# Optimization experiments

Measured on AMD Instinct MI355X. Metric: run time of the kernel, lower is better.

## Reference

```python
import jax, jax.numpy as jnp
import numpy as np

EPS = 1e-12

def _l2n(x):
    # torch F.normalize(p=2, dim=0): x / max(||x||_2, eps)
    return x / jnp.maximum(jnp.linalg.norm(x), EPS)

def _gru_cell(x, h, Wi, Wh, bi, bh):
    # torch GRU cell math; Wi:(3H,Din), Wh:(3H,H)
    gi = Wi @ x + bi
    gh = Wh @ h + bh
    i_r, i_z, i_n = jnp.split(gi, 3)
    h_r, h_z, h_n = jnp.split(gh, 3)
    r = jax.nn.sigmoid(i_r + h_r)
    z = jax.nn.sigmoid(i_z + h_z)
    n = jnp.tanh(i_n + r * h_n)
    return (1.0 - z) * n + z * h

def setup_inputs() -> dict:
    key = jax.random.key(0)
    ks = jax.random.split(key, 20)
    m, n, T = 10, 10, 100
    H1, H2, HID = 1600, 400, 2000
    D_in, D_out = 2 * m + n, m * n
    f32 = jnp.float32
    inp = {
        'y': jax.random.normal(ks[0], (n, T), f32),
        'm1x_0': jax.random.normal(ks[1], (m,), f32),
        'F': jax.random.normal(ks[2], (m, m), f32) * 0.1,
        'Hm': jax.random.normal(ks[3], (n, m), f32) * 0.1,
        'h0': jax.random.normal(ks[4], (2, HID), f32),
        'W1': jax.random.normal(ks[5], (H1, D_in), f32) * 0.05,
        'b1': jax.random.normal(ks[6], (H1,), f32) * 0.05,
        'Wi0': jax.random.normal(ks[7], (3 * HID, H1), f32) * 0.02,
        'Wh0': jax.random.normal(ks[8], (3 * HID, HID), f32) * 0.02,
        'bi0': jax.random.normal(ks[9], (3 * HID,), f32) * 0.02,
        'bh0': jax.random.normal(ks[10], (3 * HID,), f32) * 0.02,
        'Wi1': jax.random.normal(ks[11], (3 * HID, HID), f32) * 0.02,
        'Wh1': jax.random.normal(ks[12], (3 * HID, HID), f32) * 0.02,
        'bi1': jax.random.normal(ks[13], (3 * HID,), f32) * 0.02,
        'bh1': jax.random.normal(ks[14], (3 * HID,), f32) * 0.02,
        'W2': jax.random.normal(ks[15], (H2, HID), f32) * 0.02,
        'b2': jax.random.normal(ks[16], (H2,), f32) * 0.02,
        'W3': jax.random.normal(ks[17], (D_out, H2), f32) * 0.01,
        'b3': jax.random.normal(ks[18], (D_out,), f32) * 0.01,
    }
    return inp

def reference(y, m1x_0, F, Hm, h0, W1, b1, Wi0, Wh0, bi0, bh0,
              Wi1, Wh1, bi1, bh1, W2, b2, W3, b3):
    n, T = y.shape
    m = m1x_0.shape[0]
    # first step uses obs_process_0 = h(f(m1x_0)) as y_previous surrogate
    y_prev0 = Hm @ (F @ m1x_0)
    carry0 = (m1x_0, jnp.zeros_like(m1x_0), m1x_0, y_prev0, h0[0], h0[1])

    def step(carry, yt):
        post, prev_post, prev_prior, y_prev, h1, h2 = carry
        prior = F @ post              # step_prior
        m1y = Hm @ prior
        f1 = _l2n(yt - y_prev)        # innovation diff feature
        f3 = _l2n(post - prev_post)   # posterior update feature
        f4 = _l2n(post - prev_prior)  # residual feature
        kin = jnp.concatenate([f1, f3, f4])  # (2m+n,)
        a = jax.nn.relu(W1 @ kin + b1)
        h1n = _gru_cell(a, h1, Wi0, Wh0, bi0, bh0)
        h2n = _gru_cell(h1n, h2, Wi1, Wh1, bi1, bh1)
        g = jax.nn.relu(W2 @ h2n + b2)
        KG = (W3 @ g + b3).reshape(m, n)
        dy = yt - m1y
        new_post = prior + KG @ dy
        return (new_post, post, prior, yt, h1n, h2n), new_post

    _, xs = jax.lax.scan(step, carry0, y.T)  # xs: (T, m)
    return xs.T  # (m, T)
```

## Files before the change

### kernel.cpp

```cpp
#include <hip/hip_runtime.h>
#include <math.h>

#define NB 256
#define NT 1024
#define NW 16
#define TT 100
#define MM 10
#define NN 10
#define HID 2000
#define H1 1600
#define H2 400
#define G3 6000
#define KP 2048
#define RPB 24

#define SCOPE_AGENT __HIP_MEMORY_SCOPE_AGENT

typedef _Float16 h2v __attribute__((ext_vector_type(2)));

__device__ __forceinline__ float sigf(float x) { return 1.f / (1.f + __expf(-x)); }
__device__ __forceinline__ float tanhfast(float x) { return 2.f / (1.f + __expf(-2.f * x)) - 1.f; }

__device__ __forceinline__ float ld_coh(const float* p) {
  return __hip_atomic_load(p, __ATOMIC_RELAXED, SCOPE_AGENT);
}
__device__ __forceinline__ void st_coh(float* p, float v) {
  __hip_atomic_store(p, v, __ATOMIC_RELAXED, SCOPE_AGENT);
}
__device__ __forceinline__ float2 ld_coh2(const float* p) {
  unsigned long long v = __hip_atomic_load((const unsigned long long*)p,
                                           __ATOMIC_RELAXED, SCOPE_AGENT);
  union { unsigned long long u; float2 f; } c; c.u = v; return c.f;
}
__device__ __forceinline__ void stage_coh(const float* __restrict__ src,
                                          float* __restrict__ dst, int n, int tid) {
  const int n2 = n >> 1;
  for (int j = tid; j < n2; j += NT) {
    float2 v = ld_coh2(src + 2 * j);
    dst[2 * j]     = v.x;
    dst[2 * j + 1] = v.y;
  }
}

__device__ __forceinline__ void gridbar(unsigned* flags, unsigned* release,
                                        unsigned ep, int tid, int blk) {
  __syncthreads();
  if (tid == 0)
    __hip_atomic_store(flags + blk * 16, ep, __ATOMIC_RELAXED, SCOPE_AGENT);
  if (blk == 0) {
    if (tid < NB) {
      while (__hip_atomic_load(flags + tid * 16, __ATOMIC_RELAXED, SCOPE_AGENT) < ep)
        __builtin_amdgcn_s_sleep(1);
    }
    __syncthreads();
    if (tid == 0)
      __hip_atomic_store(release, ep, __ATOMIC_RELAXED, SCOPE_AGENT);
  } else {
    if (tid == 0) {
      while (__hip_atomic_load(release, __ATOMIC_RELAXED, SCOPE_AGENT) < ep)
        __builtin_amdgcn_s_sleep(1);
    }
  }
  __syncthreads();
}

__device__ __forceinline__ void set_flag(unsigned* f, unsigned v, int tid) {
  __syncthreads();
  if (tid == 0) __hip_atomic_store(f, v, __ATOMIC_RELAXED, SCOPE_AGENT);
}
__device__ __forceinline__ void wait_flag(const unsigned* f, unsigned v, int tid) {
  if (tid == 0) {
    while (__hip_atomic_load(f, __ATOMIC_RELAXED, SCOPE_AGENT) < v)
      __builtin_amdgcn_s_sleep(1);
  }
  __syncthreads();
}

template<int K>
__device__ __forceinline__ float rowdotT(const float* __restrict__ row,
                                         const float* __restrict__ x, int ln) {
  constexpr int NFULL = K / 256;
  constexpr int REM   = K - NFULL * 256;
  const int base = ln * 4;
  float4 w[NFULL + (REM ? 1 : 0)];
  #pragma unroll
  for (int i = 0; i < NFULL; ++i)
    w[i] = *reinterpret_cast<const float4*>(row + base + i * 256);
  bool tail = false;
  if constexpr (REM != 0) {
    tail = (base + NFULL * 256 + 3 < K);
    if (tail) w[NFULL] = *reinterpret_cast<const float4*>(row + base + NFULL * 256);
  }
  float acc = 0.f;
  #pragma unroll
  for (int i = 0; i < NFULL; ++i) {
    const float4 xv = *reinterpret_cast<const float4*>(x + base + i * 256);
    acc = fmaf(w[i].x, xv.x, acc);
    acc = fmaf(w[i].y, xv.y, acc);
    acc = fmaf(w[i].z, xv.z, acc);
    acc = fmaf(w[i].w, xv.w, acc);
  }
  if constexpr (REM != 0) {
    if (tail) {
      const float4 xv = *reinterpret_cast<const float4*>(x + base + NFULL * 256);
      acc = fmaf(w[NFULL].x, xv.x, acc);
      acc = fmaf(w[NFULL].y, xv.y, acc);
      acc = fmaf(w[NFULL].z, xv.z, acc);
      acc = fmaf(w[NFULL].w, xv.w, acc);
    }
  }
  #pragma unroll
  for (int off = 32; off; off >>= 1) acc += __shfl_xor(acc, off, 64);
  return acc;
}

__device__ __forceinline__ void sweep24(const _Float16* __restrict__ W,
                                        const float* __restrict__ bias,
                                        int row0, int nrows,
                                        const _Float16* __restrict__ xh,
                                        float* __restrict__ outw,
                                        bool relu,
                                        int wv, int ln, int tid, float* red,
                                        float* __restrict__ gloc)
{
  const _Float16* wp = W + (size_t)row0 * KP + wv * 3072 + ln * 8;
  uint4 w[6];
  #pragma unroll
  for (int c = 0; c < 6; ++c)
    w[c] = *reinterpret_cast<const uint4*>(wp + c * 512);
  float a0 = 0.f, a1 = 0.f;
  const int first = (3 * wv) >> 1;
  #pragma unroll
  for (int c = 0; c < 6; ++c) {
    const int flat = wv * 3072 + c * 512;
    const int sel  = (flat >> 11) - first;
    const int col  = (flat & (KP - 1)) + ln * 8;
    const uint4 xv = *reinterpret_cast<const uint4*>(xh + col);
    union { uint4 u; h2v h[4]; } wu, xu;
    wu.u = w[c]; xu.u = xv;
    float acc = sel ? a1 : a0;
    #pragma unroll
    for (int q = 0; q < 4; ++q)
      acc = __builtin_amdgcn_fdot2(wu.h[q], xu.h[q], acc, false);
    if (sel) a1 = acc; else a0 = acc;
  }
  #pragma unroll
  for (int off = 32; off; off >>= 1) {
    a0 += __shfl_xor(a0, off, 64);
    a1 += __shfl_xor(a1, off, 64);
  }
  __syncthreads();
  if (ln == 0) { red[wv * 2] = a0; red[wv * 2 + 1] = a1; }
  __syncthreads();
  if (tid < nrows) {
    const int k = tid / 3, m = tid % 3;
    float v = (m == 0) ? red[4 * k]
            : (m == 1) ? red[4 * k + 1] + red[4 * k + 2]
                       : red[4 * k + 3];
    v += bias[row0 + tid];
    if (relu) v = fmaxf(v, 0.f);
    if (gloc) gloc[tid] = v;
    st_coh(outw + row0 + tid, v);
  }
}

__global__ __launch_bounds__(256)
void convh(const float* __restrict__ src, _Float16* __restrict__ dst,
           int rows, int K, int padrows) {
  const size_t total = (size_t)padrows * KP;
  for (size_t i = (size_t)blockIdx.x * blockDim.x + threadIdx.x; i < total;
       i += (size_t)gridDim.x * blockDim.x) {
    const int r = (int)(i >> 11), c = (int)(i & (KP - 1));
    float v = (r < rows && c < K) ? src[(size_t)r * K + c] : 0.f;
    dst[i] = (_Float16)v;
  }
}
__global__ __launch_bounds__(256)
void convw1(const float* __restrict__ src, _Float16* __restrict__ dst) {
  const int i = blockIdx.x * 256 + threadIdx.x;
  const int r = i >> 5, c = i & 31;
  float v = (r < H1 && c < 30) ? src[r * 30 + c] : 0.f;
  dst[i] = (_Float16)v;
}

__global__ __launch_bounds__(NT)
void knet_f16(const float* __restrict__ y, const float* __restrict__ m1x0,
              const float* __restrict__ F, const float* __restrict__ Hm,
              const float* __restrict__ h0,
              const float* __restrict__ W1, const float* __restrict__ b1,
              const float* __restrict__ Wi0, const float* __restrict__ Wh0,
              const float* __restrict__ bi0, const float* __restrict__ bh0,
              const float* __restrict__ Wi1, const float* __restrict__ Wh1,
              const float* __restrict__ bi1, const float* __restrict__ bh1,
              const float* __restrict__ W2, const float* __restrict__ b2,
              const float* __restrict__ W3, const float* __restrict__ b3,
              float* __restrict__ out, float* __restrict__ ws)
{
  const int blk = blockIdx.x, tid = threadIdx.x;
  const int wv = tid >> 6, ln = tid & 63;

  float* a_ws     = ws;
  float* gi0_ws   = ws + 1600;
  float* gh0_ws   = ws + 7600;
  float* gi1_ws   = ws + 13600;
  float* gh1b     = ws + 19600;
  float* g_ws     = ws + 31600;
  float* vpart_ws = ws + 32000;
  unsigned* flags   = (unsigned*)(ws + 33728);
  unsigned* release = flags + 256 * 16;
  unsigned* vflag   = release + 16;
  unsigned* aflag   = vflag + 17 * 16;

  const _Float16* whbase = (const _Float16*)((const char*)ws + 152576);
  const _Float16* Wi0h = whbase;
  const _Float16* Wh0h = whbase + (size_t)G3 * KP;
  const _Float16* Wi1h = whbase + (size_t)2 * G3 * KP;
  const _Float16* Wh1h = whbase + (size_t)3 * G3 * KP;
  const _Float16* W2h  = whbase + (size_t)4 * G3 * KP;
  const _Float16* W1h  = whbase + (size_t)4 * G3 * KP + (size_t)408 * KP;

  __shared__ __align__(16) _Float16 ah[KP];
  __shared__ __align__(16) _Float16 h1h[KP];
  __shared__ __align__(16) _Float16 h2h[KP];
  __shared__ __align__(16) float h1l[HID];
  __shared__ __align__(16) float h2l[HID];
  __shared__ __align__(16) float xs[1728];
  __shared__ __align__(16) _Float16 kin_h[32];
  __shared__ float red[32];
  __shared__ float gloc_s[RPB];
  __shared__ float post_s[MM], prevpost_s[MM], prevprior_s[MM], prior_s[MM];
  __shared__ float dy_s[NN], yprev_s[NN], tmp_s[MM];
  __shared__ float d1_s[NN], d3_s[MM], d4_s[MM];
  __shared__ float kin_s[32], nrm_s[3];
  __shared__ float v_s[MM * NN], np_s[MM];

  for (int j = tid; j < HID; j += NT) {
    float v1 = h0[j], v2 = h0[HID + j];
    h1l[j] = v1; h2l[j] = v2;
    h1h[j] = (_Float16)v1; h2h[j] = (_Float16)v2;
  }
  for (int j = HID + tid; j < KP; j += NT) { h1h[j] = (_Float16)0.f; h2h[j] = (_Float16)0.f; }
  for (int j = H1 + tid; j < KP; j += NT) ah[j] = (_Float16)0.f;
  __syncthreads();

  unsigned ep = 0;

  for (int t = 0; t < TT; ++t) {
    float* gh1w = gh1b + (t & 1) * G3;
    float* gh1r = gh1b + ((t + 1) & 1) * G3;

    if (blk == NB - 1) {
      if (t > 0) {
        if (tid < 17) {
          while (__hip_atomic_load(vflag + tid * 16, __ATOMIC_RELAXED, SCOPE_AGENT) < (unsigned)t)
            __builtin_amdgcn_s_sleep(1);
        }
        __syncthreads();
        stage_coh(vpart_ws, xs, 1700, tid);
        __syncthreads();
        if (tid < MM * NN) {
          float s = b3[tid];
          #pragma unroll
          for (int k = 0; k < 17; ++k) s += xs[k * 100 + tid];
          v_s[tid] = s;
        }
        __syncthreads();
        if (tid < MM) {
          float np = prior_s[tid];
          #pragma unroll
          for (int j = 0; j < NN; ++j) np = fmaf(v_s[tid * NN + j], dy_s[j], np);
          out[tid * TT + (t - 1)] = np;
          np_s[tid] = np;
        }
        __syncthreads();
        if (tid < MM) {
          prevpost_s[tid]  = post_s[tid];
          prevprior_s[tid] = prior_s[tid];
          post_s[tid]      = np_s[tid];
        }
        __syncthreads();
      } else {
        if (tid < MM) {
          post_s[tid]      = m1x0[tid];
          prevpost_s[tid]  = 0.f;
          prevprior_s[tid] = m1x0[tid];
          float tv = 0.f;
          for (int j = 0; j < MM; ++j) tv = fmaf(F[tid * MM + j], m1x0[j], tv);
          tmp_s[tid] = tv;
        }
        __syncthreads();
        if (tid < NN) {
          float yp = 0.f;
          for (int j = 0; j < MM; ++j) yp = fmaf(Hm[tid * MM + j], tmp_s[j], yp);
          yprev_s[tid] = yp;
        }
        __syncthreads();
      }
      if (tid < MM) {
        float pr = 0.f;
        for (int j = 0; j < MM; ++j) pr = fmaf(F[tid * MM + j], post_s[j], pr);
        prior_s[tid] = pr;
      }
      __syncthreads();
      if (tid < NN) {
        float my = 0.f;
        for (int j = 0; j < MM; ++j) my = fmaf(Hm[tid * MM + j], prior_s[j], my);
        float yt = y[tid * TT + t];
        dy_s[tid] = yt - my;
        d1_s[tid] = yt - ((t == 0) ? yprev_s[tid] : y[tid * TT + (t - 1)]);
        d3_s[tid] = post_s[tid] - prevpost_s[tid];
        d4_s[tid] = post_s[tid] - prevprior_s[tid];
      }
      __syncthreads();
      if (tid == 0) {
        float n1 = 0.f, n3 = 0.f, n4 = 0.f;
        for (int j = 0; j < NN; ++j) n1 += d1_s[j] * d1_s[j];
        for (int j = 0; j < MM; ++j) { n3 += d3_s[j] * d3_s[j]; n4 += d4_s[j] * d4_s[j]; }
        nrm_s[0] = fmaxf(sqrtf(n1), 1e-12f);
        nrm_s[1] = fmaxf(sqrtf(n3), 1e-12f);
        nrm_s[2] = fmaxf(sqrtf(n4), 1e-12f);
      }
      __syncthreads();
      if (tid < NN) kin_s[tid] = d1_s[tid] / nrm_s[0];
      if (tid < MM) {
        kin_s[NN + tid]      = d3_s[tid] / nrm_s[1];
        kin_s[NN + MM + tid] = d4_s[tid] / nrm_s[2];
      }
      __syncthreads();
      if (tid < 32) kin_h[tid] = (_Float16)((tid < 30) ? kin_s[tid] : 0.f);
      __syncthreads();
      if (tid < 800) {
        const _Float16* wp = W1h + (size_t)tid * 64;
        uint4 q[8];
        #pragma unroll
        for (int c = 0; c < 8; ++c)
          q[c] = *reinterpret_cast<const uint4*>(wp + c * 8);
        const uint4* kq = reinterpret_cast<const uint4*>(kin_h);
        union { uint4 u; h2v h[4]; } kk[4], qq;
        #pragma unroll
        for (int c = 0; c < 4; ++c) kk[c].u = kq[c];
        const int r0 = 2 * tid;
        float s0 = b1[r0], s1 = b1[r0 + 1];
        #pragma unroll
        for (int c = 0; c < 4; ++c) {
          qq.u = q[c];
          #pragma unroll
          for (int p = 0; p < 4; ++p)
            s0 = __builtin_amdgcn_fdot2(qq.h[p], kk[c].h[p], s0, false);
        }
        #pragma unroll
        for (int c = 0; c < 4; ++c) {
          qq.u = q[c + 4];
          #pragma unroll
          for (int p = 0; p < 4; ++p)
            s1 = __builtin_amdgcn_fdot2(qq.h[p], kk[c].h[p], s1, false);
        }
        st_coh(a_ws + r0,     fmaxf(s0, 0.f));
        st_coh(a_ws + r0 + 1, fmaxf(s1, 0.f));
      }
      set_flag(aflag, (unsigned)(t + 1), tid);
    } else {
      if (blk >= 17) {
        if (blk <= 249) {
          sweep24(Wh0h, bh0, RPB * (blk - 17), RPB, h1h, gh0_ws, false, wv, ln, tid, red, nullptr);
        } else {
          #pragma unroll
          for (int i = 0; i < 4; ++i) {
            const int task = 233 + (blk - 250) + 5 * i;
            if (task < 250)
              sweep24(Wh0h, bh0, RPB * task, RPB, h1h, gh0_ws, false, wv, ln, tid, red, nullptr);
          }
        }
      }
      if (t > 0) {
        for (int j = tid; j < HID / 2; j += NT) {
          float2 ir = ld_coh2(gi1_ws + 2 * j),            hr = ld_coh2(gh1r + 2 * j);
          float2 iz = ld_coh2(gi1_ws + HID + 2 * j),      hz = ld_coh2(gh1r + HID + 2 * j);
          float2 in_ = ld_coh2(gi1_ws + 2 * HID + 2 * j), hn = ld_coh2(gh1r + 2 * HID + 2 * j);
          float r0 = sigf(ir.x + hr.x), r1 = sigf(ir.y + hr.y);
          float z0 = sigf(iz.x + hz.x), z1 = sigf(iz.y + hz.y);
          float n0 = tanhfast(in_.x + r0 * hn.x), n1 = tanhfast(in_.y + r1 * hn.y);
          float o0 = (1.f - z0) * n0 + z0 * h2l[2 * j];
          float o1 = (1.f - z1) * n1 + z1 * h2l[2 * j + 1];
          h2l[2 * j] = o0; h2l[2 * j + 1] = o1;
          h2h[2 * j] = (_Float16)o0; h2h[2 * j + 1] = (_Float16)o1;
        }
        __syncthreads();
        if (blk < 17) {
          const int row0 = RPB * blk;
          const int nr = (H2 - row0 < RPB) ? (H2 - row0) : RPB;
          sweep24(W2h, b2, row0, nr, h2h, g_ws, true, wv, ln, tid, red, gloc_s);
          __syncthreads();
          if (tid < MM * NN) {
            float s = 0.f;
            const float* w3c = W3 + (size_t)tid * H2 + row0;
            for (int j = 0; j < nr; ++j) s = fmaf(w3c[j], gloc_s[j], s);
            st_coh(vpart_ws + blk * 100 + tid, s);
          }
          set_flag(vflag + blk * 16, (unsigned)t, tid);
        }
      }
      if (blk <= 249)
        sweep24(Wh1h, bh1, RPB * blk, RPB, h2h, gh1w, false, wv, ln, tid, red, nullptr);
      if (blk <= 249) {
        wait_flag(aflag, (unsigned)(t + 1), tid);
        const int n2 = H1 >> 1;
        for (int j = tid; j < n2; j += NT) {
          float2 v = ld_coh2(a_ws + 2 * j);
          ah[2 * j]     = (_Float16)v.x;
          ah[2 * j + 1] = (_Float16)v.y;
        }
        __syncthreads();
        sweep24(Wi0h, bi0, RPB * blk, RPB, ah, gi0_ws, false, wv, ln, tid, red, nullptr);
      }
    }
    ++ep; gridbar(flags, release, ep, tid, blk);

    if (blk != NB - 1) {
      for (int j = tid; j < HID / 2; j += NT) {
        float2 ir = ld_coh2(gi0_ws + 2 * j),            hr = ld_coh2(gh0_ws + 2 * j);
        float2 iz = ld_coh2(gi0_ws + HID + 2 * j),      hz = ld_coh2(gh0_ws + HID + 2 * j);
        float2 in_ = ld_coh2(gi0_ws + 2 * HID + 2 * j), hn = ld_coh2(gh0_ws + 2 * HID + 2 * j);
        float r0 = sigf(ir.x + hr.x), r1 = sigf(ir.y + hr.y);
        float z0 = sigf(iz.x + hz.x), z1 = sigf(iz.y + hz.y);
        float n0 = tanhfast(in_.x + r0 * hn.x), n1 = tanhfast(in_.y + r1 * hn.y);
        float o0 = (1.f - z0) * n0 + z0 * h1l[2 * j];
        float o1 = (1.f - z1) * n1 + z1 * h1l[2 * j + 1];
        h1l[2 * j] = o0; h1l[2 * j + 1] = o1;
        h1h[2 * j] = (_Float16)o0; h1h[2 * j + 1] = (_Float16)o1;
      }
      __syncthreads();
      if (blk <= 249)
        sweep24(Wi1h, bi1, RPB * blk, RPB, h1h, gi1_ws, false, wv, ln, tid, red, nullptr);
    }
    ++ep; gridbar(flags, release, ep, tid, blk);
  }

  if (blk < 17) {
    float* gh1r = gh1b + ((TT + 1) & 1) * G3;
    for (int j = tid; j < HID / 2; j += NT) {
      float2 ir = ld_coh2(gi1_ws + 2 * j),            hr = ld_coh2(gh1r + 2 * j);
      float2 iz = ld_coh2(gi1_ws + HID + 2 * j),      hz = ld_coh2(gh1r + HID + 2 * j);
      float2 in_ = ld_coh2(gi1_ws + 2 * HID + 2 * j), hn = ld_coh2(gh1r + 2 * HID + 2 * j);
      float r0 = sigf(ir.x + hr.x), r1 = sigf(ir.y + hr.y);
      float z0 = sigf(iz.x + hz.x), z1 = sigf(iz.y + hz.y);
      float n0 = tanhfast(in_.x + r0 * hn.x), n1 = tanhfast(in_.y + r1 * hn.y);
      float o0 = (1.f - z0) * n0 + z0 * h2l[2 * j];
      float o1 = (1.f - z1) * n1 + z1 * h2l[2 * j + 1];
      h2h[2 * j] = (_Float16)o0; h2h[2 * j + 1] = (_Float16)o1;
    }
    __syncthreads();
    const int row0 = RPB * blk;
    const int nr = (H2 - row0 < RPB) ? (H2 - row0) : RPB;
    sweep24(W2h, b2, row0, nr, h2h, g_ws, true, wv, ln, tid, red, gloc_s);
    __syncthreads();
    if (tid < MM * NN) {
      float s = 0.f;
      const float* w3c = W3 + (size_t)tid * H2 + row0;
      for (int j = 0; j < nr; ++j) s = fmaf(w3c[j], gloc_s[j], s);
      st_coh(vpart_ws + blk * 100 + tid, s);
    }
    set_flag(vflag + blk * 16, (unsigned)TT, tid);
  }
  if (blk == NB - 1) {
    if (tid < 17) {
      while (__hip_atomic_load(vflag + tid * 16, __ATOMIC_RELAXED, SCOPE_AGENT) < (unsigned)TT)
        __builtin_amdgcn_s_sleep(1);
    }
    __syncthreads();
    stage_coh(vpart_ws, xs, 1700, tid);
    __syncthreads();
    if (tid < MM * NN) {
      float s = b3[tid];
      #pragma unroll
      for (int k = 0; k < 17; ++k) s += xs[k * 100 + tid];
      v_s[tid] = s;
    }
    __syncthreads();
    if (tid < MM) {
      float np = prior_s[tid];
      #pragma unroll
      for (int j = 0; j < NN; ++j) np = fmaf(v_s[tid * NN + j], dy_s[j], np);
      out[tid * TT + (TT - 1)] = np;
    }
  }
}

__global__ __launch_bounds__(NT)
void knet_f32(const float* __restrict__ y, const float* __restrict__ m1x0,
              const float* __restrict__ F, const float* __restrict__ Hm,
              const float* __restrict__ h0,
              const float* __restrict__ W1, const float* __restrict__ b1,
              const float* __restrict__ Wi0, const float* __restrict__ Wh0,
              const float* __restrict__ bi0, const float* __restrict__ bh0,
              const float* __restrict__ Wi1, const float* __restrict__ Wh1,
              const float* __restrict__ bi1, const float* __restrict__ bh1,
              const float* __restrict__ W2, const float* __restrict__ b2,
              const float* __restrict__ W3, const float* __restrict__ b3,
              float* __restrict__ out, float* __restrict__ ws)
{
  const int blk = blockIdx.x, tid = threadIdx.x;
  const int wv = tid >> 6, ln = tid & 63;

  float* a_ws   = ws;
  float* gi0_ws = ws + 1600;
  float* gh0_ws = ws + 7600;
  float* gi1_ws = ws + 13600;
  float* gh1_ws = ws + 19600;
  float* g_ws   = ws + 25600;
  unsigned* flags   = (unsigned*)(ws + 26624);
  unsigned* release = flags + NB * 16;

  __shared__ __align__(16) float xs[1664];
  __shared__ __align__(16) float h1l[HID];
  __shared__ __align__(16) float h2l[HID];
  __shared__ float post_s[MM], prevpost_s[MM], prevprior_s[MM], prior_s[MM];
  __shared__ float dy_s[NN], yprev_s[NN], tmp_s[MM];
  __shared__ float d1_s[NN], d3_s[MM], d4_s[MM];
  __shared__ float kin_s[32], nrm_s[3];
  __shared__ float v_s[MM * NN], np_s[MM];

  for (int j = tid; j < HID; j += NT) { h1l[j] = h0[j]; h2l[j] = h0[HID + j]; }
  __syncthreads();

  unsigned ep = 0;

  for (int t = 0; t < TT; ++t) {
    if (blk == NB - 1) {
      if (t > 0) {
        stage_coh(g_ws, xs, H2, tid);
        __syncthreads();
        for (int r = wv; r < MM * NN; r += NW) {
          float acc = rowdotT<H2>(W3 + (size_t)r * H2, xs, ln);
          if (ln == 0) v_s[r] = acc + b3[r];
        }
        __syncthreads();
        if (tid < MM) {
          float np = prior_s[tid];
          #pragma unroll
          for (int j = 0; j < NN; ++j) np = fmaf(v_s[tid * NN + j], dy_s[j], np);
          out[tid * TT + (t - 1)] = np;
          np_s[tid] = np;
        }
        __syncthreads();
        if (tid < MM) {
          prevpost_s[tid]  = post_s[tid];
          prevprior_s[tid] = prior_s[tid];
          post_s[tid]      = np_s[tid];
        }
        __syncthreads();
      } else {
        if (tid < MM) {
          post_s[tid]      = m1x0[tid];
          prevpost_s[tid]  = 0.f;
          prevprior_s[tid] = m1x0[tid];
          float tv = 0.f;
          for (int j = 0; j < MM; ++j) tv = fmaf(F[tid * MM + j], m1x0[j], tv);
          tmp_s[tid] = tv;
        }
        __syncthreads();
        if (tid < NN) {
          float yp = 0.f;
          for (int j = 0; j < MM; ++j) yp = fmaf(Hm[tid * MM + j], tmp_s[j], yp);
          yprev_s[tid] = yp;
        }
        __syncthreads();
      }
      if (tid < MM) {
        float pr = 0.f;
        for (int j = 0; j < MM; ++j) pr = fmaf(F[tid * MM + j], post_s[j], pr);
        prior_s[tid] = pr;
      }
      __syncthreads();
      if (tid < NN) {
        float my = 0.f;
        for (int j = 0; j < MM; ++j) my = fmaf(Hm[tid * MM + j], prior_s[j], my);
        float yt = y[tid * TT + t];
        dy_s[tid] = yt - my;
        d1_s[tid] = yt - ((t == 0) ? yprev_s[tid] : y[tid * TT + (t - 1)]);
        d3_s[tid] = post_s[tid] - prevpost_s[tid];
        d4_s[tid] = post_s[tid] - prevprior_s[tid];
      }
      __syncthreads();
      if (tid == 0) {
        float n1 = 0.f, n3 = 0.f, n4 = 0.f;
        for (int j = 0; j < NN; ++j) n1 += d1_s[j] * d1_s[j];
        for (int j = 0; j < MM; ++j) { n3 += d3_s[j] * d3_s[j]; n4 += d4_s[j] * d4_s[j]; }
        nrm_s[0] = fmaxf(sqrtf(n1), 1e-12f);
        nrm_s[1] = fmaxf(sqrtf(n3), 1e-12f);
        nrm_s[2] = fmaxf(sqrtf(n4), 1e-12f);
      }
      __syncthreads();
      if (tid < NN) kin_s[tid] = d1_s[tid] / nrm_s[0];
      if (tid < MM) {
        kin_s[NN + tid]      = d3_s[tid] / nrm_s[1];
        kin_s[NN + MM + tid] = d4_s[tid] / nrm_s[2];
      }
      __syncthreads();
      for (int r = tid; r < H1; r += NT) {
        float acc = b1[r];
        const float* row = W1 + (size_t)r * 30;
        #pragma unroll
        for (int k = 0; k < 30; ++k) acc = fmaf(row[k], kin_s[k], acc);
        st_coh(a_ws + r, fmaxf(acc, 0.f));
      }
    } else {
      const int gw = blk * NW + wv;
      for (int r = gw; r < G3; r += (NB - 1) * NW) {
        float acc = rowdotT<HID>(Wh1 + (size_t)r * HID, h2l, ln);
        if (ln == 0) st_coh(gh1_ws + r, acc + bh1[r]);
      }
      if (t == 0) {
        for (int r = gw; r < G3; r += (NB - 1) * NW) {
          float acc = rowdotT<HID>(Wh0 + (size_t)r * HID, h1l, ln);
          if (ln == 0) st_coh(gh0_ws + r, acc + bh0[r]);
        }
      }
    }
    ++ep; gridbar(flags, release, ep, tid, blk);

    stage_coh(a_ws, xs, H1, tid);
    __syncthreads();
    {
      const int gw = blk * NW + wv;
      for (int r = gw; r < G3; r += NB * NW) {
        float acc = rowdotT<H1>(Wi0 + (size_t)r * H1, xs, ln);
        if (ln == 0) st_coh(gi0_ws + r, acc + bi0[r]);
      }
    }
    ++ep; gridbar(flags, release, ep, tid, blk);

    {
      for (int j = tid; j < HID / 2; j += NT) {
        float2 ir = ld_coh2(gi0_ws + 2 * j),            hr = ld_coh2(gh0_ws + 2 * j);
        float2 iz = ld_coh2(gi0_ws + HID + 2 * j),      hz = ld_coh2(gh0_ws + HID + 2 * j);
        float2 in_ = ld_coh2(gi0_ws + 2 * HID + 2 * j), hn = ld_coh2(gh0_ws + 2 * HID + 2 * j);
        float r0 = sigf(ir.x + hr.x), r1 = sigf(ir.y + hr.y);
        float z0 = sigf(iz.x + hz.x), z1 = sigf(iz.y + hz.y);
        float n0 = tanhfast(in_.x + r0 * hn.x), n1 = tanhfast(in_.y + r1 * hn.y);
        h1l[2 * j]     = (1.f - z0) * n0 + z0 * h1l[2 * j];
        h1l[2 * j + 1] = (1.f - z1) * n1 + z1 * h1l[2 * j + 1];
      }
      __syncthreads();
      const int gw = blk * NW + wv;
      for (int r = gw; r < G3; r += NB * NW) {
        float acc = rowdotT<HID>(Wi1 + (size_t)r * HID, h1l, ln);
        if (ln == 0) st_coh(gi1_ws + r, acc + bi1[r]);
      }
    }
    ++ep; gridbar(flags, release, ep, tid, blk);

    {
      for (int j = tid; j < HID / 2; j += NT) {
        float2 ir = ld_coh2(gi1_ws + 2 * j),            hr = ld_coh2(gh1_ws + 2 * j);
        float2 iz = ld_coh2(gi1_ws + HID + 2 * j),      hz = ld_coh2(gh1_ws + HID + 2 * j);
        float2 in_ = ld_coh2(gi1_ws + 2 * HID + 2 * j), hn = ld_coh2(gh1_ws + 2 * HID + 2 * j);
        float r0 = sigf(ir.x + hr.x), r1 = sigf(ir.y + hr.y);
        float z0 = sigf(iz.x + hz.x), z1 = sigf(iz.y + hz.y);
        float n0 = tanhfast(in_.x + r0 * hn.x), n1 = tanhfast(in_.y + r1 * hn.y);
        h2l[2 * j]     = (1.f - z0) * n0 + z0 * h2l[2 * j];
        h2l[2 * j + 1] = (1.f - z1) * n1 + z1 * h2l[2 * j + 1];
      }
      __syncthreads();
      const int gw = blk * NW + wv;
      for (int r = gw; r < H2 + G3; r += NB * NW) {
        if (r < H2) {
          float acc = rowdotT<HID>(W2 + (size_t)r * HID, h2l, ln);
          if (ln == 0) st_coh(g_ws + r, fmaxf(acc + b2[r], 0.f));
        } else {
          const int rr = r - H2;
          float acc = rowdotT<HID>(Wh0 + (size_t)rr * HID, h1l, ln);
          if (ln == 0) st_coh(gh0_ws + rr, acc + bh0[rr]);
        }
      }
    }
    ++ep; gridbar(flags, release, ep, tid, blk);
  }

  if (blk == NB - 1) {
    stage_coh(g_ws, xs, H2, tid);
    __syncthreads();
    for (int r = wv; r < MM * NN; r += NW) {
      float acc = rowdotT<H2>(W3 + (size_t)r * H2, xs, ln);
      if (ln == 0) v_s[r] = acc + b3[r];
    }
    __syncthreads();
    if (tid < MM) {
      float np = prior_s[tid];
      #pragma unroll
      for (int j = 0; j < NN; ++j) np = fmaf(v_s[tid * NN + j], dy_s[j], np);
      out[tid * TT + (TT - 1)] = np;
    }
  }
}

extern "C" void kernel_launch(void* const* d_in, const int* in_sizes, int n_in,
                              void* d_out, int out_size, void* d_ws, size_t ws_size,
                              hipStream_t stream) {
  const float* y    = (const float*)d_in[0];
  const float* m1x0 = (const float*)d_in[1];
  const float* F    = (const float*)d_in[2];
  const float* Hm   = (const float*)d_in[3];
  const float* h0   = (const float*)d_in[4];
  const float* W1   = (const float*)d_in[5];
  const float* b1   = (const float*)d_in[6];
  const float* Wi0  = (const float*)d_in[7];
  const float* Wh0  = (const float*)d_in[8];
  const float* bi0  = (const float*)d_in[9];
  const float* bh0  = (const float*)d_in[10];
  const float* Wi1  = (const float*)d_in[11];
  const float* Wh1  = (const float*)d_in[12];
  const float* bi1  = (const float*)d_in[13];
  const float* bh1  = (const float*)d_in[14];
  const float* W2   = (const float*)d_in[15];
  const float* b2   = (const float*)d_in[16];
  const float* W3   = (const float*)d_in[17];
  const float* b3   = (const float*)d_in[18];
  float* out = (float*)d_out;
  float* ws  = (float*)d_ws;

  const size_t WBASE = 152576;
  const size_t NEED = WBASE +
      ((size_t)4 * G3 * KP + (size_t)408 * KP + (size_t)65536) * 2;

  void* args[] = { &y, &m1x0, &F, &Hm, &h0, &W1, &b1, &Wi0, &Wh0, &bi0, &bh0,
                   &Wi1, &Wh1, &bi1, &bh1, &W2, &b2, &W3, &b3, &out, &ws };

  if (ws_size >= NEED) {
    hipMemsetAsync((char*)d_ws + 33728 * sizeof(float), 0, 275 * 64, stream);
    _Float16* wh = (_Float16*)((char*)d_ws + WBASE);
    convh<<<2048, 256, 0, stream>>>(Wi0, wh,                         G3, H1,  G3);
    convh<<<2048, 256, 0, stream>>>(Wh0, wh + (size_t)G3 * KP,       G3, HID, G3);
    convh<<<2048, 256, 0, stream>>>(Wi1, wh + (size_t)2 * G3 * KP,   G3, HID, G3);
    convh<<<2048, 256, 0, stream>>>(Wh1, wh + (size_t)3 * G3 * KP,   G3, HID, G3);
    convh<<<2048, 256, 0, stream>>>(W2,  wh + (size_t)4 * G3 * KP,   H2, HID, 408);
    convw1<<<256, 256, 0, stream>>>(W1,  wh + (size_t)4 * G3 * KP + (size_t)408 * KP);
    hipLaunchCooperativeKernel((const void*)knet_f16, dim3(NB), dim3(NT),
                               args, 0, stream);
  } else {
    hipMemsetAsync((char*)d_ws + 26624 * sizeof(float), 0, NB * 64 + 64, stream);
    hipLaunchCooperativeKernel((const void*)knet_f32, dim3(NB), dim3(NT),
                               args, 0, stream);
  }
}
```

Measured before the change: 3.733 ms.

## Rebalance GRU sweeps to 48 rows per block and replicate W1 layer locally

Each block now handles 48 rows per sweep instead of 24, with three rows per wave sharing one staged x vector. Work is reassigned so each matrix (Wh0, Wi0, Wi1, Wh1, W2) is covered by about 125 blocks. The serial block now only publishes the packed kin vector, and every Wi0 block recomputes the small W1 layer locally. That removes the a_ws round trip and the f32-to-f16 staging, and drops the gh1 double buffer. Blocks only recompute the GRU states they actually consume. The cost is redundant W1 compute on many blocks and longer per-block sweeps on fewer active blocks.

```diff
diff --git a/kernel.cpp b/kernel.cpp
--- a/kernel.cpp
+++ b/kernel.cpp
@@ -12,7 +12,8 @@
 #define H2 400
 #define G3 6000
 #define KP 2048
-#define RPB 24
+#define RPB 48
+#define NTASK 125
 
 #define SCOPE_AGENT __HIP_MEMORY_SCOPE_AGENT
 
@@ -21,9 +22,6 @@
 __device__ __forceinline__ float sigf(float x) { return 1.f / (1.f + __expf(-x)); }
 __device__ __forceinline__ float tanhfast(float x) { return 2.f / (1.f + __expf(-2.f * x)) - 1.f; }
 
-__device__ __forceinline__ float ld_coh(const float* p) {
-  return __hip_atomic_load(p, __ATOMIC_RELAXED, SCOPE_AGENT);
-}
 __device__ __forceinline__ void st_coh(float* p, float v) {
   __hip_atomic_store(p, v, __ATOMIC_RELAXED, SCOPE_AGENT);
 }
@@ -31,6 +29,12 @@
   unsigned long long v = __hip_atomic_load((const unsigned long long*)p,
                                            __ATOMIC_RELAXED, SCOPE_AGENT);
   union { unsigned long long u; float2 f; } c; c.u = v; return c.f;
+}
+__device__ __forceinline__ unsigned ld_coh_u32(const unsigned* p) {
+  return __hip_atomic_load(p, __ATOMIC_RELAXED, SCOPE_AGENT);
+}
+__device__ __forceinline__ void st_coh_u32(unsigned* p, unsigned v) {
+  __hip_atomic_store(p, v, __ATOMIC_RELAXED, SCOPE_AGENT);
 }
 __device__ __forceinline__ void stage_coh(const float* __restrict__ src,
                                           float* __restrict__ dst, int n, int tid) {
@@ -114,53 +118,58 @@
   return acc;
 }
 
-__device__ __forceinline__ void sweep24(const _Float16* __restrict__ W,
+__device__ __forceinline__ void sweep48(const _Float16* __restrict__ W,
                                         const float* __restrict__ bias,
                                         int row0, int nrows,
                                         const _Float16* __restrict__ xh,
-                                        float* __restrict__ outw,
-                                        bool relu,
+                                        float* __restrict__ outw, bool relu,
                                         int wv, int ln, int tid, float* red,
                                         float* __restrict__ gloc)
 {
-  const _Float16* wp = W + (size_t)row0 * KP + wv * 3072 + ln * 8;
-  uint4 w[6];
+  const _Float16* wp = W + (size_t)(row0 + 3 * wv) * KP + ln * 8;
+  uint4 xv[4];
   #pragma unroll
-  for (int c = 0; c < 6; ++c)
-    w[c] = *reinterpret_cast<const uint4*>(wp + c * 512);
-  float a0 = 0.f, a1 = 0.f;
-  const int first = (3 * wv) >> 1;
+  for (int c = 0; c < 4; ++c)
+    xv[c] = *reinterpret_cast<const uint4*>(xh + c * 512 + ln * 8);
+  uint4 w[12];
   #pragma unroll
-  for (int c = 0; c < 6; ++c) {
-    const int flat = wv * 3072 + c * 512;
-    const int sel  = (flat >> 11) - first;
-    const int col  = (flat & (KP - 1)) + ln * 8;
-    const uint4 xv = *reinterpret_cast<const uint4*>(xh + col);
-    union { uint4 u; h2v h[4]; } wu, xu;
-    wu.u = w[c]; xu.u = xv;
-    float acc = sel ? a1 : a0;
+  for (int r = 0; r < 3; ++r)
     #pragma unroll
-    for (int q = 0; q < 4; ++q)
-      acc = __builtin_amdgcn_fdot2(wu.h[q], xu.h[q], acc, false);
-    if (sel) a1 = acc; else a0 = acc;
+    for (int c = 0; c < 4; ++c)
+      w[r * 4 + c] = *reinterpret_cast<const uint4*>(wp + (size_t)r * KP + c * 512);
+  float a0 = 0.f, a1 = 0.f, a2 = 0.f;
+  union U { uint4 u; h2v h[4]; };
+  #pragma unroll
+  for (int c = 0; c < 4; ++c) {
+    U xu; xu.u = xv[c];
+    U w0; w0.u = w[c];
+    U w1; w1.u = w[4 + c];
+    U w2; w2.u = w[8 + c];
+    #pragma unroll
+    for (int q = 0; q < 4; ++q) {
+      a0 = __builtin_amdgcn_fdot2(w0.h[q], xu.h[q], a0, false);
+      a1 = __builtin_amdgcn_fdot2(w1.h[q], xu.h[q], a1, false);
+      a2 = __builtin_amdgcn_fdot2(w2.h[q], xu.h[q], a2, false);
+    }
   }
   #pragma unroll
   for (int off = 32; off; off >>= 1) {
     a0 += __shfl_xor(a0, off, 64);
     a1 += __shfl_xor(a1, off, 64);
+    a2 += __shfl_xor(a2, off, 64);
   }
   __syncthreads();
-  if (ln == 0) { red[wv * 2] = a0; red[wv * 2 + 1] = a1; }
+  if (ln == 0) {
+    red[wv * 3]     = a0;
+    red[wv * 3 + 1] = a1;
+    red[wv * 3 + 2] = a2;
+  }
   __syncthreads();
   if (tid < nrows) {
-    const int k = tid / 3, m = tid % 3;
-    float v = (m == 0) ? red[4 * k]
-            : (m == 1) ? red[4 * k + 1] + red[4 * k + 2]
-                       : red[4 * k + 3];
-    v += bias[row0 + tid];
+    float v = red[tid] + bias[row0 + tid];
     if (relu) v = fmaxf(v, 0.f);
     if (gloc) gloc[tid] = v;
-    st_coh(outw + row0 + tid, v);
+    if (outw) st_coh(outw + row0 + tid, v);
   }
 }
 
@@ -199,34 +208,33 @@
   const int blk = blockIdx.x, tid = threadIdx.x;
   const int wv = tid >> 6, ln = tid & 63;
 
-  float* a_ws     = ws;
-  float* gi0_ws   = ws + 1600;
-  float* gh0_ws   = ws + 7600;
-  float* gi1_ws   = ws + 13600;
-  float* gh1b     = ws + 19600;
-  float* g_ws     = ws + 31600;
-  float* vpart_ws = ws + 32000;
-  unsigned* flags   = (unsigned*)(ws + 33728);
+  float* gi0_ws   = ws;
+  float* gh0_ws   = ws + 6000;
+  float* gi1_ws   = ws + 12000;
+  float* gh1_ws   = ws + 18000;
+  float* vpart_ws = ws + 24000;
+  unsigned* kinpack = (unsigned*)(ws + 24928);
+  unsigned* flags   = (unsigned*)(ws + 25024);
   unsigned* release = flags + 256 * 16;
   unsigned* vflag   = release + 16;
-  unsigned* aflag   = vflag + 17 * 16;
-
-  const _Float16* whbase = (const _Float16*)((const char*)ws + 152576);
+  unsigned* kflag   = vflag + 9 * 16;
+
+  const _Float16* whbase = (const _Float16*)((const char*)ws + 131072);
   const _Float16* Wi0h = whbase;
   const _Float16* Wh0h = whbase + (size_t)G3 * KP;
   const _Float16* Wi1h = whbase + (size_t)2 * G3 * KP;
   const _Float16* Wh1h = whbase + (size_t)3 * G3 * KP;
   const _Float16* W2h  = whbase + (size_t)4 * G3 * KP;
-  const _Float16* W1h  = whbase + (size_t)4 * G3 * KP + (size_t)408 * KP;
+  const _Float16* W1h  = whbase + (size_t)4 * G3 * KP + (size_t)432 * KP;
 
   __shared__ __align__(16) _Float16 ah[KP];
   __shared__ __align__(16) _Float16 h1h[KP];
   __shared__ __align__(16) _Float16 h2h[KP];
   __shared__ __align__(16) float h1l[HID];
   __shared__ __align__(16) float h2l[HID];
-  __shared__ __align__(16) float xs[1728];
+  __shared__ __align__(16) float xs[1024];
   __shared__ __align__(16) _Float16 kin_h[32];
-  __shared__ float red[32];
+  __shared__ float red[RPB];
   __shared__ float gloc_s[RPB];
   __shared__ float post_s[MM], prevpost_s[MM], prevprior_s[MM], prior_s[MM];
   __shared__ float dy_s[NN], yprev_s[NN], tmp_s[MM];
@@ -243,25 +251,30 @@
   for (int j = H1 + tid; j < KP; j += NT) ah[j] = (_Float16)0.f;
   __syncthreads();
 
+  const bool isSerial = (blk == NB - 1);
+  const bool roleW2   = (blk < 9);
+  const bool roleWh0  = (blk >= 9 && blk < 134);
+  const bool roleWi0  = (!isSerial) && (blk >= 134 || (blk >= 5 && blk < 9));
+  const int  wi0task  = (blk >= 134) ? (blk - 134) : (121 + (blk - 5));
+  const bool needC2   = roleW2 || (blk >= 125 && blk < 250);
+  const bool needC1   = (!isSerial) && (blk < 134);
+
   unsigned ep = 0;
 
   for (int t = 0; t < TT; ++t) {
-    float* gh1w = gh1b + (t & 1) * G3;
-    float* gh1r = gh1b + ((t + 1) & 1) * G3;
-
-    if (blk == NB - 1) {
+    if (isSerial) {
       if (t > 0) {
-        if (tid < 17) {
+        if (tid < 9) {
           while (__hip_atomic_load(vflag + tid * 16, __ATOMIC_RELAXED, SCOPE_AGENT) < (unsigned)t)
             __builtin_amdgcn_s_sleep(1);
         }
         __syncthreads();
-        stage_coh(vpart_ws, xs, 1700, tid);
+        stage_coh(vpart_ws, xs, 900, tid);
         __syncthreads();
         if (tid < MM * NN) {
           float s = b3[tid];
           #pragma unroll
-          for (int k = 0; k < 17; ++k) s += xs[k * 100 + tid];
+          for (int k = 0; k < 9; ++k) s += xs[k * 100 + tid];
           v_s[tid] = s;
         }
         __syncthreads();
@@ -329,54 +342,16 @@
       __syncthreads();
       if (tid < 32) kin_h[tid] = (_Float16)((tid < 30) ? kin_s[tid] : 0.f);
       __syncthreads();
-      if (tid < 800) {
-        const _Float16* wp = W1h + (size_t)tid * 64;
-        uint4 q[8];
-        #pragma unroll
-        for (int c = 0; c < 8; ++c)
-          q[c] = *reinterpret_cast<const uint4*>(wp + c * 8);
-        const uint4* kq = reinterpret_cast<const uint4*>(kin_h);
-        union { uint4 u; h2v h[4]; } kk[4], qq;
-        #pragma unroll
-        for (int c = 0; c < 4; ++c) kk[c].u = kq[c];
-        const int r0 = 2 * tid;
-        float s0 = b1[r0], s1 = b1[r0 + 1];
-        #pragma unroll
-        for (int c = 0; c < 4; ++c) {
-          qq.u = q[c];
-          #pragma unroll
-          for (int p = 0; p < 4; ++p)
-            s0 = __builtin_amdgcn_fdot2(qq.h[p], kk[c].h[p], s0, false);
-        }
-        #pragma unroll
-        for (int c = 0; c < 4; ++c) {
-          qq.u = q[c + 4];
-          #pragma unroll
-          for (int p = 0; p < 4; ++p)
-            s1 = __builtin_amdgcn_fdot2(qq.h[p], kk[c].h[p], s1, false);
-        }
-        st_coh(a_ws + r0,     fmaxf(s0, 0.f));
-        st_coh(a_ws + r0 + 1, fmaxf(s1, 0.f));
-      }
-      set_flag(aflag, (unsigned)(t + 1), tid);
+      if (tid < 16) st_coh_u32(kinpack + tid, ((const unsigned*)kin_h)[tid]);
+      set_flag(kflag, (unsigned)(t + 1), tid);
     } else {
-      if (blk >= 17) {
-        if (blk <= 249) {
-          sweep24(Wh0h, bh0, RPB * (blk - 17), RPB, h1h, gh0_ws, false, wv, ln, tid, red, nullptr);
-        } else {
-          #pragma unroll
-          for (int i = 0; i < 4; ++i) {
-            const int task = 233 + (blk - 250) + 5 * i;
-            if (task < 250)
-              sweep24(Wh0h, bh0, RPB * task, RPB, h1h, gh0_ws, false, wv, ln, tid, red, nullptr);
-          }
-        }
-      }
-      if (t > 0) {
+      if (roleWh0)
+        sweep48(Wh0h, bh0, RPB * (blk - 9), RPB, h1h, gh0_ws, false, wv, ln, tid, red, nullptr);
+      if (t > 0 && needC2) {
         for (int j = tid; j < HID / 2; j += NT) {
-          float2 ir = ld_coh2(gi1_ws + 2 * j),            hr = ld_coh2(gh1r + 2 * j);
-          float2 iz = ld_coh2(gi1_ws + HID + 2 * j),      hz = ld_coh2(gh1r + HID + 2 * j);
-          float2 in_ = ld_coh2(gi1_ws + 2 * HID + 2 * j), hn = ld_coh2(gh1r + 2 * HID + 2 * j);
+          float2 ir = ld_coh2(gi1_ws + 2 * j),            hr = ld_coh2(gh1_ws + 2 * j);
+          float2 iz = ld_coh2(gi1_ws + HID + 2 * j),      hz = ld_coh2(gh1_ws + HID + 2 * j);
+          float2 in_ = ld_coh2(gi1_ws + 2 * HID + 2 * j), hn = ld_coh2(gh1_ws + 2 * HID + 2 * j);
           float r0 = sigf(ir.x + hr.x), r1 = sigf(ir.y + hr.y);
           float z0 = sigf(iz.x + hz.x), z1 = sigf(iz.y + hz.y);
           float n0 = tanhfast(in_.x + r0 * hn.x), n1 = tanhfast(in_.y + r1 * hn.y);
@@ -386,62 +361,89 @@
           h2h[2 * j] = (_Float16)o0; h2h[2 * j + 1] = (_Float16)o1;
         }
         __syncthreads();
-        if (blk < 17) {
-          const int row0 = RPB * blk;
-          const int nr = (H2 - row0 < RPB) ? (H2 - row0) : RPB;
-          sweep24(W2h, b2, row0, nr, h2h, g_ws, true, wv, ln, tid, red, gloc_s);
-          __syncthreads();
-          if (tid < MM * NN) {
-            float s = 0.f;
-            const float* w3c = W3 + (size_t)tid * H2 + row0;
-            for (int j = 0; j < nr; ++j) s = fmaf(w3c[j], gloc_s[j], s);
-            st_coh(vpart_ws + blk * 100 + tid, s);
+      }
+      if (t > 0 && roleW2) {
+        const int row0 = RPB * blk;
+        const int nr = (H2 - row0 < RPB) ? (H2 - row0) : RPB;
+        sweep48(W2h, b2, row0, nr, h2h, nullptr, true, wv, ln, tid, red, gloc_s);
+        __syncthreads();
+        if (tid < MM * NN) {
+          float s = 0.f;
+          const float* w3c = W3 + (size_t)tid * H2 + row0;
+          for (int j = 0; j < nr; ++j) s = fmaf(w3c[j], gloc_s[j], s);
+          st_coh(vpart_ws + blk * 100 + tid, s);
+        }
+        set_flag(vflag + blk * 16, (unsigned)t, tid);
+      }
+      if (roleWi0) {
+        wait_flag(kflag, (unsigned)(t + 1), tid);
+        if (tid < 16) ((unsigned*)kin_h)[tid] = ld_coh_u32(kinpack + tid);
+        __syncthreads();
+        if (tid < 800) {
+          const _Float16* wp = W1h + (size_t)tid * 64;
+          uint4 q[8];
+          #pragma unroll
+          for (int c = 0; c < 8; ++c)
+            q[c] = *reinterpret_cast<const uint4*>(wp + c * 8);
+          const uint4* kq = reinterpret_cast<const uint4*>(kin_h);
+          union U { uint4 u; h2v h[4]; };
+          U kk[4];
+          #pragma unroll
+          for (int c = 0; c < 4; ++c) kk[c].u = kq[c];
+          const int r0 = 2 * tid;
+          float s0 = b1[r0], s1 = b1[r0 + 1];
+          #pragma unroll
+          for (int c = 0; c < 4; ++c) {
+            U qq; qq.u = q[c];
+            #pragma unroll
+            for (int p = 0; p < 4; ++p)
+              s0 = __builtin_amdgcn_fdot2(qq.h[p], kk[c].h[p], s0, false);
           }
-          set_flag(vflag + blk * 16, (unsigned)t, tid);
-        }
-      }
-      if (blk <= 249)
-        sweep24(Wh1h, bh1, RPB * blk, RPB, h2h, gh1w, false, wv, ln, tid, red, nullptr);
-      if (blk <= 249) {
-        wait_flag(aflag, (unsigned)(t + 1), tid);
-        const int n2 = H1 >> 1;
-        for (int j = tid; j < n2; j += NT) {
-          float2 v = ld_coh2(a_ws + 2 * j);
-          ah[2 * j]     = (_Float16)v.x;
-          ah[2 * j + 1] = (_Float16)v.y;
-        }
-        __syncthreads();
-        sweep24(Wi0h, bi0, RPB * blk, RPB, ah, gi0_ws, false, wv, ln, tid, red, nullptr);
+          #pragma unroll
+          for (int c = 0; c < 4; ++c) {
+            U qq; qq.u = q[c + 4];
+            #pragma unroll
+            for (int p = 0; p < 4; ++p)
+              s1 = __builtin_amdgcn_fdot2(qq.h[p], kk[c].h[p], s1, false);
+          }
+          ah[r0]     = (_Float16)fmaxf(s0, 0.f);
+          ah[r0 + 1] = (_Float16)fmaxf(s1, 0.f);
+        }
+        __syncthreads();
+        sweep48(Wi0h, bi0, RPB * wi0task, RPB, ah, gi0_ws, false, wv, ln, tid, red, nullptr);
       }
     }
     ++ep; gridbar(flags, release, ep, tid, blk);
 
-    if (blk != NB - 1) {
-      for (int j = tid; j < HID / 2; j += NT) {
-        float2 ir = ld_coh2(gi0_ws + 2 * j),            hr = ld_coh2(gh0_ws + 2 * j);
-        float2 iz = ld_coh2(gi0_ws + HID + 2 * j),      hz = ld_coh2(gh0_ws + HID + 2 * j);
-        float2 in_ = ld_coh2(gi0_ws + 2 * HID + 2 * j), hn = ld_coh2(gh0_ws + 2 * HID + 2 * j);
-        float r0 = sigf(ir.x + hr.x), r1 = sigf(ir.y + hr.y);
-        float z0 = sigf(iz.x + hz.x), z1 = sigf(iz.y + hz.y);
-        float n0 = tanhfast(in_.x + r0 * hn.x), n1 = tanhfast(in_.y + r1 * hn.y);
-        float o0 = (1.f - z0) * n0 + z0 * h1l[2 * j];
-        float o1 = (1.f - z1) * n1 + z1 * h1l[2 * j + 1];
-        h1l[2 * j] = o0; h1l[2 * j + 1] = o1;
-        h1h[2 * j] = (_Float16)o0; h1h[2 * j + 1] = (_Float16)o1;
-      }
-      __syncthreads();
-      if (blk <= 249)
-        sweep24(Wi1h, bi1, RPB * blk, RPB, h1h, gi1_ws, false, wv, ln, tid, red, nullptr);
+    if (!isSerial) {
+      if (needC1) {
+        for (int j = tid; j < HID / 2; j += NT) {
+          float2 ir = ld_coh2(gi0_ws + 2 * j),            hr = ld_coh2(gh0_ws + 2 * j);
+          float2 iz = ld_coh2(gi0_ws + HID + 2 * j),      hz = ld_coh2(gh0_ws + HID + 2 * j);
+          float2 in_ = ld_coh2(gi0_ws + 2 * HID + 2 * j), hn = ld_coh2(gh0_ws + 2 * HID + 2 * j);
+          float r0 = sigf(ir.x + hr.x), r1 = sigf(ir.y + hr.y);
+          float z0 = sigf(iz.x + hz.x), z1 = sigf(iz.y + hz.y);
+          float n0 = tanhfast(in_.x + r0 * hn.x), n1 = tanhfast(in_.y + r1 * hn.y);
+          float o0 = (1.f - z0) * n0 + z0 * h1l[2 * j];
+          float o1 = (1.f - z1) * n1 + z1 * h1l[2 * j + 1];
+          h1l[2 * j] = o0; h1l[2 * j + 1] = o1;
+          h1h[2 * j] = (_Float16)o0; h1h[2 * j + 1] = (_Float16)o1;
+        }
+        __syncthreads();
+      }
+      if (blk < 125)
+        sweep48(Wi1h, bi1, RPB * blk, RPB, h1h, gi1_ws, false, wv, ln, tid, red, nullptr);
+      else if (blk < 250)
+        sweep48(Wh1h, bh1, RPB * (blk - 125), RPB, h2h, gh1_ws, false, wv, ln, tid, red, nullptr);
     }
     ++ep; gridbar(flags, release, ep, tid, blk);
   }
 
-  if (blk < 17) {
-    float* gh1r = gh1b + ((TT + 1) & 1) * G3;
+  if (roleW2) {
     for (int j = tid; j < HID / 2; j += NT) {
-      float2 ir = ld_coh2(gi1_ws + 2 * j),            hr = ld_coh2(gh1r + 2 * j);
-      float2 iz = ld_coh2(gi1_ws + HID + 2 * j),      hz = ld_coh2(gh1r + HID + 2 * j);
-      float2 in_ = ld_coh2(gi1_ws + 2 * HID + 2 * j), hn = ld_coh2(gh1r + 2 * HID + 2 * j);
+      float2 ir = ld_coh2(gi1_ws + 2 * j),            hr = ld_coh2(gh1_ws + 2 * j);
+      float2 iz = ld_coh2(gi1_ws + HID + 2 * j),      hz = ld_coh2(gh1_ws + HID + 2 * j);
+      float2 in_ = ld_coh2(gi1_ws + 2 * HID + 2 * j), hn = ld_coh2(gh1_ws + 2 * HID + 2 * j);
       float r0 = sigf(ir.x + hr.x), r1 = sigf(ir.y + hr.y);
       float z0 = sigf(iz.x + hz.x), z1 = sigf(iz.y + hz.y);
       float n0 = tanhfast(in_.x + r0 * hn.x), n1 = tanhfast(in_.y + r1 * hn.y);
@@ -452,7 +454,7 @@
     __syncthreads();
     const int row0 = RPB * blk;
     const int nr = (H2 - row0 < RPB) ? (H2 - row0) : RPB;
-    sweep24(W2h, b2, row0, nr, h2h, g_ws, true, wv, ln, tid, red, gloc_s);
+    sweep48(W2h, b2, row0, nr, h2h, nullptr, true, wv, ln, tid, red, gloc_s);
     __syncthreads();
     if (tid < MM * NN) {
       float s = 0.f;
@@ -462,18 +464,18 @@
     }
     set_flag(vflag + blk * 16, (unsigned)TT, tid);
   }
-  if (blk == NB - 1) {
-    if (tid < 17) {
+  if (isSerial) {
+    if (tid < 9) {
       while (__hip_atomic_load(vflag + tid * 16, __ATOMIC_RELAXED, SCOPE_AGENT) < (unsigned)TT)
         __builtin_amdgcn_s_sleep(1);
     }
     __syncthreads();
-    stage_coh(vpart_ws, xs, 1700, tid);
+    stage_coh(vpart_ws, xs, 900, tid);
     __syncthreads();
     if (tid < MM * NN) {
       float s = b3[tid];
       #pragma unroll
-      for (int k = 0; k < 17; ++k) s += xs[k * 100 + tid];
+      for (int k = 0; k < 9; ++k) s += xs[k * 100 + tid];
       v_s[tid] = s;
     }
     __syncthreads();
@@ -719,22 +721,22 @@
   float* out = (float*)d_out;
   float* ws  = (float*)d_ws;
 
-  const size_t WBASE = 152576;
+  const size_t WBASE = 131072;
   const size_t NEED = WBASE +
-      ((size_t)4 * G3 * KP + (size_t)408 * KP + (size_t)65536) * 2;
+      ((size_t)4 * G3 * KP + (size_t)432 * KP + (size_t)65536) * 2;
 
   void* args[] = { &y, &m1x0, &F, &Hm, &h0, &W1, &b1, &Wi0, &Wh0, &bi0, &bh0,
                    &Wi1, &Wh1, &bi1, &bh1, &W2, &b2, &W3, &b3, &out, &ws };
 
   if (ws_size >= NEED) {
-    hipMemsetAsync((char*)d_ws + 33728 * sizeof(float), 0, 275 * 64, stream);
+    hipMemsetAsync((char*)d_ws + 25024 * sizeof(float), 0, 4272 * 4, stream);
     _Float16* wh = (_Float16*)((char*)d_ws + WBASE);
     convh<<<2048, 256, 0, stream>>>(Wi0, wh,                         G3, H1,  G3);
     convh<<<2048, 256, 0, stream>>>(Wh0, wh + (size_t)G3 * KP,       G3, HID, G3);
     convh<<<2048, 256, 0, stream>>>(Wi1, wh + (size_t)2 * G3 * KP,   G3, HID, G3);
     convh<<<2048, 256, 0, stream>>>(Wh1, wh + (size_t)3 * G3 * KP,   G3, HID, G3);
-    convh<<<2048, 256, 0, stream>>>(W2,  wh + (size_t)4 * G3 * KP,   H2, HID, 408);
-    convw1<<<256, 256, 0, stream>>>(W1,  wh + (size_t)4 * G3 * KP + (size_t)408 * KP);
+    convh<<<2048, 256, 0, stream>>>(W2,  wh + (size_t)4 * G3 * KP,   H2, HID, 432);
+    convw1<<<256, 256, 0, stream>>>(W1,  wh + (size_t)4 * G3 * KP + (size_t)432 * KP);
     hipLaunchCooperativeKernel((const void*)knet_f16, dim3(NB), dim3(NT),
                                args, 0, stream);
   } else {
```

After: 4.209 ms. +12.8%, slower.
